# Kernel optimization log

Hardware: AMD Instinct MI355X
Metric: run time of the kernel (lower is better)

## Reference

```python
import jax, jax.numpy as jnp
import numpy as np

B = 256
D = 2048          # in_channels (shared latent dim)
S = 8             # n_subjects
OUT = 1000        # sum of 7 Schaefer network head widths [150,148,132,136,76,122,236]


def setup_inputs() -> dict:
    key = jax.random.key(0)
    k1, k2, k3, k4 = jax.random.split(key, 4)
    x = jax.random.normal(k1, (B, D), dtype=jnp.float32)
    subject_ids = jax.random.randint(k2, (B,), 0, S, dtype=jnp.int64)
    scale = 1.0 / np.sqrt(D)  # matches normal_(0, 1/in_channels**0.5)
    # Concatenated per-head weights: equivalent to 7 heads of shapes
    # (S, D, n_k) concatenated along the output axis (n_k sums to OUT).
    W = jax.random.normal(k3, (S, D, OUT), dtype=jnp.float32) * scale
    b = jax.random.normal(k4, (S, OUT), dtype=jnp.float32) * scale
    return {"x": x, "subject_ids": subject_ids, "W": W, "b": b}


def reference(x, subject_ids, W, b):
    # Per-sample weight gather (B, D, OUT) followed by batched matmul,
    # exactly mirroring torch: w = weights[subject_ids]; einsum('bd,bdo->bo').
    w = W[subject_ids]                      # (B, D, OUT) gathered copy
    out = jnp.einsum('bd,bdo->bo', x, w)    # (B, OUT)
    out = out + b[subject_ids]              # per-subject bias
    return out
```

## Files before the change

### kernel.cpp

```cpp
#include <hip/hip_runtime.h>
#include <stdint.h>

#define Bn   256
#define Dn   2048
#define Sn   8
#define ON   1000

#define ROWS 64
#define OT   256
#define KS   256
#define NDC  (Dn / KS)
#define STK  32
#define NST  (KS / STK)
#define LDKS 40
#define BUFB (OT * LDKS * 2)

typedef short v8s __attribute__((ext_vector_type(8)));
typedef short v4s __attribute__((ext_vector_type(4)));
typedef float v4f __attribute__((ext_vector_type(4)));

static __device__ __forceinline__ short f2bf(float f) {
    union { float f; uint32_t u; } v; v.f = f;
    uint32_t u = v.u;
    u += 0x7FFFu + ((u >> 16) & 1u);
    return (short)(u >> 16);
}

__global__ __launch_bounds__(512) void main_kernel(const float* __restrict__ x,
                                                   const int* __restrict__ sid,
                                                   const float* __restrict__ W,
                                                   float* __restrict__ part) {
    __shared__ unsigned short Bsh[2][OT * LDKS];
    __shared__ unsigned long long bmask[8];
    __shared__ int rows_l[ROWS];

    const int oc = blockIdx.x;
    const int kc = blockIdx.y;
    const int s  = blockIdx.z;
    const int o0 = oc * OT;
    const int k0 = kc * KS;
    const int t  = threadIdx.x;
    const int lane = t & 63;
    const int w    = t >> 6;

    const int mysid = (t < Bn) ? sid[t] : -1;
    const bool match = (mysid == s);
    const unsigned long long m = __ballot(match);
    if (lane == 0) bmask[w] = m;
    if (t < ROWS) rows_l[t] = -1;
    __syncthreads();
    if (match) {
        int pos = __popcll(m & ((1ull << lane) - 1ull));
        for (int ww = 0; ww < w; ++ww) pos += __popcll(bmask[ww]);
        if (pos < ROWS) rows_l[pos] = t;
    }
    __syncthreads();

    int og = o0 + 4 * lane;
    if (og > ON - 4) og = ON - 4;
    const float* wpb = W + ((size_t)s * Dn + k0 + 4 * w) * ON + og;

    unsigned short* wr[4];
#pragma unroll
    for (int i = 0; i < 4; ++i)
        wr[i] = (unsigned short*)((char*)&Bsh[0][0]
                + (4 * lane + i) * 80 + 16 * ((w >> 1) ^ (lane & 3)) + 8 * (w & 1));

    const int lo16 = lane & 15;
    const int quad = lane >> 4;
    const int arow = (w >> 1) * 16 + lo16;
    const int xrow = rows_l[arow];
    const bool wactive = (rows_l[(w >> 1) * 16] >= 0);
    const float* xp = (xrow >= 0 ? x + (size_t)xrow * Dn : x) + k0 + quad * 8;

    float4 a0[NST], a1[NST];
#pragma unroll
    for (int st = 0; st < NST; ++st) {
        a0[st] = *(const float4*)(xp + st * STK);
        a1[st] = *(const float4*)(xp + st * STK + 4);
    }

    v4f fb[3][4];
#pragma unroll
    for (int c = 0; c < 3; ++c)
#pragma unroll
        for (int r = 0; r < 4; ++r)
            fb[c][r] = *(const v4f*)(wpb + ((size_t)c * STK + r) * ON);

    v8s af[NST];
#pragma unroll
    for (int st = 0; st < NST; ++st) {
        v8s a;
        a[0] = f2bf(a0[st].x); a[1] = f2bf(a0[st].y);
        a[2] = f2bf(a0[st].z); a[3] = f2bf(a0[st].w);
        a[4] = f2bf(a1[st].x); a[5] = f2bf(a1[st].y);
        a[6] = f2bf(a1[st].z); a[7] = f2bf(a1[st].w);
        af[st] = a;
    }

    const int rb0  = (w & 1) * 128 + lo16;
    const int rswz = 16 * (quad ^ ((lo16 >> 2) & 3));

    v4f acc[8];
#pragma unroll
    for (int i = 0; i < 8; ++i) acc[i] = (v4f){0.f, 0.f, 0.f, 0.f};

#pragma unroll
    for (int st = 0; st < NST; ++st) {
        const int sl = st & 1;
        const int rg = st % 3;
#pragma unroll
        for (int i = 0; i < 4; ++i) {
            v4s kv;
            kv[0] = f2bf(fb[rg][0][i]);
            kv[1] = f2bf(fb[rg][1][i]);
            kv[2] = f2bf(fb[rg][2][i]);
            kv[3] = f2bf(fb[rg][3][i]);
            *(v4s*)((char*)wr[i] + sl * BUFB) = kv;
        }
        if (st + 3 < NST) {
#pragma unroll
            for (int r = 0; r < 4; ++r)
                fb[rg][r] = *(const v4f*)(wpb + ((size_t)(st + 3) * STK + r) * ON);
        }
        asm volatile("s_waitcnt lgkmcnt(0)" ::: "memory");
        __builtin_amdgcn_s_barrier();
        asm volatile("" ::: "memory");

        if (wactive) {
            const v8s a = af[st];
            const char* bb = (const char*)&Bsh[sl][0];
#pragma unroll
            for (int nt = 0; nt < 8; ++nt) {
                const v8s bf = *(const v8s*)(bb + (rb0 + nt * 16) * 80 + rswz);
                acc[nt] = __builtin_amdgcn_mfma_f32_16x16x32_bf16(a, bf, acc[nt],
                                                                  0, 0, 0);
            }
        }
    }

    if (wactive) {
        float* pp = part + (size_t)kc * Bn * ON;
        const int er0 = (w >> 1) * 16 + quad * 4;
#pragma unroll
        for (int nt = 0; nt < 8; ++nt) {
            const int o = o0 + (w & 1) * 128 + nt * 16 + lo16;
            if (o < ON) {
#pragma unroll
                for (int r = 0; r < 4; ++r) {
                    const int bi = rows_l[er0 + r];
                    if (bi >= 0) pp[(size_t)bi * ON + o] = acc[nt][r];
                }
            }
        }
    }
}

__global__ __launch_bounds__(256) void reduce_kernel(const int* __restrict__ sid,
                                                     const float* __restrict__ bias,
                                                     const float* __restrict__ part,
                                                     float* __restrict__ out) {
    const int b = blockIdx.x;
    const int s = sid[b];
    const int o = threadIdx.x * 4;
    if (o < ON) {
        float4 v = *(const float4*)(bias + (size_t)s * ON + o);
#pragma unroll
        for (int d = 0; d < NDC; d++) {
            const float4 p = *(const float4*)(part + ((size_t)d * Bn + b) * ON + o);
            v.x += p.x; v.y += p.y; v.z += p.z; v.w += p.w;
        }
        *(float4*)(out + (size_t)b * ON + o) = v;
    }
}

extern "C" void kernel_launch(void* const* d_in, const int* in_sizes, int n_in,
                              void* d_out, int out_size, void* d_ws, size_t ws_size,
                              hipStream_t stream) {
    const float* x    = (const float*)d_in[0];
    const int*   sid  = (const int*)d_in[1];
    const float* W    = (const float*)d_in[2];
    const float* bias = (const float*)d_in[3];
    float*       out  = (float*)d_out;
    float*       part = (float*)d_ws;

    main_kernel<<<dim3(4, NDC, Sn), dim3(512), 0, stream>>>(x, sid, W, part);
    reduce_kernel<<<dim3(Bn), dim3(256), 0, stream>>>(sid, bias, part, out);
}
```

Baseline: 107.3 us.

## Stage most K-steps into separate LDS buffers to cut per-step barriers

```diff
diff --git a/kernel.cpp b/kernel.cpp
--- a/kernel.cpp
+++ b/kernel.cpp
@@ -12,8 +12,9 @@
 #define NDC  (Dn / KS)
 #define STK  32
 #define NST  (KS / STK)
+#define NBUF 7
 #define LDKS 40
-#define BUFB (OT * LDKS * 2)
+#define SUBB (OT * LDKS * 2)
 
 typedef short v8s __attribute__((ext_vector_type(8)));
 typedef short v4s __attribute__((ext_vector_type(4)));
@@ -30,7 +31,7 @@
                                                    const int* __restrict__ sid,
                                                    const float* __restrict__ W,
                                                    float* __restrict__ part) {
-    __shared__ unsigned short Bsh[2][OT * LDKS];
+    __shared__ unsigned short Bsh[NBUF][OT * LDKS];
     __shared__ unsigned long long bmask[8];
     __shared__ int rows_l[ROWS];
 
@@ -106,8 +107,7 @@
     for (int i = 0; i < 8; ++i) acc[i] = (v4f){0.f, 0.f, 0.f, 0.f};
 
 #pragma unroll
-    for (int st = 0; st < NST; ++st) {
-        const int sl = st & 1;
+    for (int st = 0; st < NBUF; ++st) {
         const int rg = st % 3;
 #pragma unroll
         for (int i = 0; i < 4; ++i) {
@@ -116,20 +116,48 @@
             kv[1] = f2bf(fb[rg][1][i]);
             kv[2] = f2bf(fb[rg][2][i]);
             kv[3] = f2bf(fb[rg][3][i]);
-            *(v4s*)((char*)wr[i] + sl * BUFB) = kv;
+            *(v4s*)((char*)wr[i] + st * SUBB) = kv;
         }
         if (st + 3 < NST) {
 #pragma unroll
             for (int r = 0; r < 4; ++r)
                 fb[rg][r] = *(const v4f*)(wpb + ((size_t)(st + 3) * STK + r) * ON);
         }
-        asm volatile("s_waitcnt lgkmcnt(0)" ::: "memory");
-        __builtin_amdgcn_s_barrier();
-        asm volatile("" ::: "memory");
-
-        if (wactive) {
+    }
+    asm volatile("s_waitcnt lgkmcnt(0)" ::: "memory");
+    __builtin_amdgcn_s_barrier();
+    asm volatile("" ::: "memory");
+
+    if (wactive) {
+        const v8s a = af[0];
+        const char* bb = (const char*)&Bsh[0][0];
+#pragma unroll
+        for (int nt = 0; nt < 8; ++nt) {
+            const v8s bf = *(const v8s*)(bb + (rb0 + nt * 16) * 80 + rswz);
+            acc[nt] = __builtin_amdgcn_mfma_f32_16x16x32_bf16(a, bf, acc[nt], 0, 0, 0);
+        }
+    }
+    __builtin_amdgcn_s_barrier();
+    asm volatile("" ::: "memory");
+
+#pragma unroll
+    for (int i = 0; i < 4; ++i) {
+        v4s kv;
+        kv[0] = f2bf(fb[1][0][i]);
+        kv[1] = f2bf(fb[1][1][i]);
+        kv[2] = f2bf(fb[1][2][i]);
+        kv[3] = f2bf(fb[1][3][i]);
+        *(v4s*)((char*)wr[i]) = kv;
+    }
+    asm volatile("s_waitcnt lgkmcnt(0)" ::: "memory");
+    __builtin_amdgcn_s_barrier();
+    asm volatile("" ::: "memory");
+
+    if (wactive) {
+#pragma unroll
+        for (int st = 1; st < NST; ++st) {
             const v8s a = af[st];
-            const char* bb = (const char*)&Bsh[sl][0];
+            const char* bb = (const char*)&Bsh[(st < NBUF) ? st : 0][0];
 #pragma unroll
             for (int nt = 0; nt < 8; ++nt) {
                 const v8s bf = *(const v8s*)(bb + (rb0 + nt * 16) * 80 + rswz);
```

Result: no change. 108.4 us (+1.0%).

## Fuse split-K reduction into main kernel using inter-block flag synchronization

Applied to the files above, without the earlier changes.

```diff
diff --git a/kernel.cpp b/kernel.cpp
--- a/kernel.cpp
+++ b/kernel.cpp
@@ -14,6 +14,7 @@
 #define NST  (KS / STK)
 #define LDKS 40
 #define BUFB (OT * LDKS * 2)
+#define MAGIC 0x13579BDFu
 
 typedef short v8s __attribute__((ext_vector_type(8)));
 typedef short v4s __attribute__((ext_vector_type(4)));
@@ -29,7 +30,10 @@
 __global__ __launch_bounds__(512) void main_kernel(const float* __restrict__ x,
                                                    const int* __restrict__ sid,
                                                    const float* __restrict__ W,
-                                                   float* __restrict__ part) {
+                                                   const float* __restrict__ bias,
+                                                   float* __restrict__ part,
+                                                   unsigned int* __restrict__ flags,
+                                                   float* __restrict__ out) {
     __shared__ unsigned short Bsh[2][OT * LDKS];
     __shared__ unsigned long long bmask[8];
     __shared__ int rows_l[ROWS];
@@ -154,23 +158,30 @@
             }
         }
     }
-}
-
-__global__ __launch_bounds__(256) void reduce_kernel(const int* __restrict__ sid,
-                                                     const float* __restrict__ bias,
-                                                     const float* __restrict__ part,
-                                                     float* __restrict__ out) {
-    const int b = blockIdx.x;
-    const int s = sid[b];
-    const int o = threadIdx.x * 4;
-    if (o < ON) {
-        float4 v = *(const float4*)(bias + (size_t)s * ON + o);
-#pragma unroll
-        for (int d = 0; d < NDC; d++) {
-            const float4 p = *(const float4*)(part + ((size_t)d * Bn + b) * ON + o);
-            v.x += p.x; v.y += p.y; v.z += p.z; v.w += p.w;
-        }
-        *(float4*)(out + (size_t)b * ON + o) = v;
+
+    unsigned int* flg = flags + (oc * Sn + s) * NDC;
+    __threadfence();
+    __syncthreads();
+    if (t == 0) atomicExch(&flg[kc], MAGIC);
+    if (t < NDC) {
+        while (atomicAdd(&flg[t], 0u) != MAGIC) __builtin_amdgcn_s_sleep(8);
+    }
+    __syncthreads();
+    __threadfence();
+
+    {
+        const int rr = t >> 3;
+        const int o  = o0 + kc * 32 + (t & 7) * 4;
+        const int bi = rows_l[rr];
+        if (bi >= 0 && o <= ON - 4) {
+            float4 v = *(const float4*)(bias + (size_t)s * ON + o);
+#pragma unroll
+            for (int d = 0; d < NDC; ++d) {
+                const float4 p = *(const float4*)(part + ((size_t)d * Bn + bi) * ON + o);
+                v.x += p.x; v.y += p.y; v.z += p.z; v.w += p.w;
+            }
+            *(float4*)(out + (size_t)bi * ON + o) = v;
+        }
     }
 }
 
@@ -183,7 +194,9 @@
     const float* bias = (const float*)d_in[3];
     float*       out  = (float*)d_out;
     float*       part = (float*)d_ws;
-
-    main_kernel<<<dim3(4, NDC, Sn), dim3(512), 0, stream>>>(x, sid, W, part);
-    reduce_kernel<<<dim3(Bn), dim3(256), 0, stream>>>(sid, bias, part, out);
+    unsigned int* flags = (unsigned int*)((char*)d_ws
+                        + (size_t)NDC * Bn * ON * sizeof(float));
+
+    main_kernel<<<dim3(4, NDC, Sn), dim3(512), 0, stream>>>(x, sid, W, bias,
+                                                            part, flags, out);
 }
```

After: 211.6 us. 97.1% more time.
